# Optimization experiments

Hardware: AMD Instinct MI355X
Metric: run time of the kernel (lower is better)

## Reference

```python
import jax, jax.numpy as jnp
import numpy as np

DIM = 512
HEADS = 8
LANDMARKS = 64


def setup_inputs() -> dict:
    key = jax.random.key(0)
    ks = jax.random.split(key, 9)
    B, N, C = 2, 16384, DIM
    s = 0.02
    return {
        "x": jax.random.normal(ks[0], (B, N, C), dtype=jnp.float32),
        "wq": jax.random.normal(ks[1], (C, C), dtype=jnp.float32) * s,
        "bq": jnp.zeros((C,), dtype=jnp.float32),
        "wk": jax.random.normal(ks[2], (C, C), dtype=jnp.float32) * s,
        "bk": jnp.zeros((C,), dtype=jnp.float32),
        "wv": jax.random.normal(ks[3], (C, C), dtype=jnp.float32) * s,
        "bv": jnp.zeros((C,), dtype=jnp.float32),
        "wo": jax.random.normal(ks[4], (C, C), dtype=jnp.float32) * s,
        "bo": jnp.zeros((C,), dtype=jnp.float32),
    }


def _to_heads(x, H):
    B, N, C = x.shape
    return x.reshape(B, N, H, C // H).transpose(0, 2, 1, 3)  # (B,H,N,hd)


def reference(x, wq, bq, wk, bk, wv, bv, wo, bo):
    B, N, C = x.shape
    H = HEADS
    hd = C // H
    scale = hd ** (-0.5)
    m = min(LANDMARKS, N)

    q = _to_heads(x @ wq.T + bq, H) * scale  # (B,H,N,hd)
    k = _to_heads(x @ wk.T + bk, H)
    v = _to_heads(x @ wv.T + bv, H)

    if N <= m * 2:
        attn = jax.nn.softmax(jnp.einsum("bhnd,bhkd->bhnk", q, k), axis=-1)
        out = jnp.einsum("bhnk,bhkd->bhnd", attn, v)
    else:
        seg = (N + m - 1) // m
        pad = seg * m - N
        if pad > 0:
            q_p = jnp.pad(q, ((0, 0), (0, 0), (0, pad), (0, 0)))
            k_p = jnp.pad(k, ((0, 0), (0, 0), (0, pad), (0, 0)))
        else:
            q_p, k_p = q, k
        # landmarks: mean over consecutive segments of length seg (zero-pad included, as in torch)
        q_land = q_p.reshape(B, H, m, seg, hd).mean(3)  # (B,H,m,hd)
        k_land = k_p.reshape(B, H, m, seg, hd).mean(3)

        ker1 = jax.nn.softmax(jnp.einsum("bhnd,bhmd->bhnm", q, k_land), axis=-1)  # (B,H,N,m)
        ker2 = jax.nn.softmax(jnp.einsum("bhld,bhmd->bhlm", q_land, k_land), axis=-1)  # (B,H,m,m)
        ker3 = jax.nn.softmax(jnp.einsum("bhmd,bhnd->bhmn", q_land, k), axis=-1)  # (B,H,m,N)
        ker2_inv = jnp.linalg.pinv(ker2)  # (B,H,m,m)

        kv = jnp.einsum("bhmn,bhnd->bhmd", ker3, v)  # (B,H,m,hd)
        out = jnp.einsum("bhnm,bhmd->bhnd", ker1, ker2_inv @ kv)

    out = out.transpose(0, 2, 1, 3).reshape(B, N, C)
    return out @ wo.T + bo
```

## Files before the change

kernel.cpp:

```cpp
#include <hip/hip_runtime.h>
#include <stdint.h>


constexpr int B_   = 2;
constexpr int N_   = 16384;
constexpr int C_   = 512;
constexpr int H_   = 8;
constexpr int HD_  = 64;
constexpr int LM_  = 64;
constexpr int SEG_ = 256;
constexpr int BH_  = 16;
constexpr int NCH_ = 16;
constexpr int NPART_ = 64;
constexpr int SW1_ = 3;
constexpr int SW2_ = 2;

#define RCOND_ (640.0 * 1.1920928955078125e-07)

typedef unsigned short ushort4_t __attribute__((ext_vector_type(4)));
typedef unsigned short ushort8_t __attribute__((ext_vector_type(8)));
typedef __bf16 bf16x8 __attribute__((ext_vector_type(8)));
typedef float f32x4 __attribute__((ext_vector_type(4)));

__device__ inline float bf2f(unsigned short u) {
  union { unsigned int i; float f; } x; x.i = ((unsigned int)u) << 16; return x.f;
}
__device__ inline unsigned short f2bf(float f) {
  union { float f; unsigned int i; } x; x.f = f;
  unsigned int lsb = (x.i >> 16) & 1;
  return (unsigned short)((x.i + 0x7fffu + lsb) >> 16);
}
__device__ inline bf16x8 ld_bf8(const unsigned short* p) { return *(const bf16x8*)p; }

__device__ __forceinline__ void gload_lds16(const unsigned short* gsrc, unsigned short* ldst) {
  __builtin_amdgcn_global_load_lds((const __attribute__((address_space(1))) void*)gsrc,
                                   (__attribute__((address_space(3))) void*)ldst, 16, 0, 0);
}

__global__ __launch_bounds__(256) void cvt_bf16_kernel(const float* __restrict__ src,
                                                       unsigned short* __restrict__ dst,
                                                       int n8) {
  int i = (blockIdx.x * 256 + threadIdx.x);
  if (i >= n8) return;
  const float* s = src + (size_t)i * 8;
  float4 x0 = *(const float4*)(s);
  float4 x1 = *(const float4*)(s + 4);
  ushort8_t u;
  u[0] = f2bf(x0.x); u[1] = f2bf(x0.y); u[2] = f2bf(x0.z); u[3] = f2bf(x0.w);
  u[4] = f2bf(x1.x); u[5] = f2bf(x1.y); u[6] = f2bf(x1.z); u[7] = f2bf(x1.w);
  *(ushort8_t*)(dst + (size_t)i * 8) = u;
}

__global__ __launch_bounds__(256) void seg_mean_kernel(const float* __restrict__ x,
                                                       float* __restrict__ xbar) {
  int bl = blockIdx.x;
  int b = bl / LM_, l = bl % LM_;
  int t = threadIdx.x;
  int c4 = t & 127;
  int rh = t >> 7;
  const float* xp = x + ((size_t)b * N_ + (size_t)l * SEG_) * C_;
  float4 s = make_float4(0.f, 0.f, 0.f, 0.f);
  for (int r = rh * 128; r < rh * 128 + 128; ++r) {
    float4 v = *(const float4*)(xp + (size_t)r * C_ + c4 * 4);
    s.x += v.x; s.y += v.y; s.z += v.z; s.w += v.w;
  }
  __shared__ float red[2][512];
  *(float4*)&red[rh][c4 * 4] = s;
  __syncthreads();
  if (rh == 0) {
    float4 a = *(float4*)&red[0][c4 * 4];
    float4 c = *(float4*)&red[1][c4 * 4];
    const float invs = 1.0f / SEG_;
    float4 o;
    o.x = (a.x + c.x) * invs; o.y = (a.y + c.y) * invs;
    o.z = (a.z + c.z) * invs; o.w = (a.w + c.w) * invs;
    *(float4*)(xbar + (size_t)bl * C_ + c4 * 4) = o;
  }
}

__global__ __launch_bounds__(256) void land_gemm_kernel(const float* __restrict__ xbar,
                                                        const float* __restrict__ wq,
                                                        const float* __restrict__ bq,
                                                        const float* __restrict__ wk,
                                                        const float* __restrict__ bk,
                                                        float* __restrict__ qland,
                                                        float* __restrict__ kland,
                                                        unsigned short* __restrict__ qlbh,
                                                        unsigned short* __restrict__ qlbl,
                                                        unsigned short* __restrict__ klb) {
  __shared__ float As[32][68];
  __shared__ float Ws[32][68];
  int which = blockIdx.x >> 1;
  int row0 = (blockIdx.x & 1) * 64;
  int col0 = blockIdx.y * 64;
  const float* A = xbar;
  const float* W = which ? wk : wq;
  const float* bias = which ? bk : bq;
  float scale = which ? 1.0f : 0.125f;
  float* out = which ? kland : qland;
  int tid = threadIdx.x;
  int tm = tid >> 4, tn = tid & 15;
  float acc[4][4] = {};
  for (int k0 = 0; k0 < C_; k0 += 32) {
#pragma unroll
    for (int i = 0; i < 2; ++i) {
      int s = tid + i * 256;
      int r = s >> 3;
      int kg = (s & 7) << 2;
      float4 av = *(const float4*)(A + (size_t)(row0 + r) * C_ + k0 + kg);
      As[kg + 0][r] = av.x; As[kg + 1][r] = av.y;
      As[kg + 2][r] = av.z; As[kg + 3][r] = av.w;
      float4 wv = *(const float4*)(W + (size_t)(col0 + r) * C_ + k0 + kg);
      Ws[kg + 0][r] = wv.x; Ws[kg + 1][r] = wv.y;
      Ws[kg + 2][r] = wv.z; Ws[kg + 3][r] = wv.w;
    }
    __syncthreads();
#pragma unroll
    for (int kk = 0; kk < 32; ++kk) {
      float4 a = *(const float4*)&As[kk][tm * 4];
      float4 b = *(const float4*)&Ws[kk][tn * 4];
      float av[4] = {a.x, a.y, a.z, a.w};
      float bv[4] = {b.x, b.y, b.z, b.w};
#pragma unroll
      for (int i = 0; i < 4; ++i)
#pragma unroll
        for (int j = 0; j < 4; ++j) acc[i][j] += av[i] * bv[j];
    }
    __syncthreads();
  }
#pragma unroll
  for (int i = 0; i < 4; ++i) {
    int row = row0 + tm * 4 + i;
    int d0 = tn * 4;
    float o4[4];
#pragma unroll
    for (int j = 0; j < 4; ++j) o4[j] = (acc[i][j] + bias[col0 + d0 + j]) * scale;
    int b = row / LM_, n = row % LM_;
    int h = col0 >> 6;
    size_t idx = (((size_t)(b * H_ + h) * LM_) + n) * HD_ + d0;
    float4 o; o.x = o4[0]; o.y = o4[1]; o.z = o4[2]; o.w = o4[3];
    *(float4*)(out + idx) = o;
    if (which == 0) {
      ushort4_t uh, ul;
#pragma unroll
      for (int j = 0; j < 4; ++j) {
        unsigned short hbits = f2bf(o4[j]);
        uh[j] = hbits;
        ul[j] = f2bf(o4[j] - bf2f(hbits));
      }
      *(ushort4_t*)(qlbh + idx) = uh;
      *(ushort4_t*)(qlbl + idx) = ul;
    } else {
      ushort4_t uk;
#pragma unroll
      for (int j = 0; j < 4; ++j) uk[j] = f2bf(o4[j]);
      *(ushort4_t*)(klb + idx) = uk;
    }
  }
}

__device__ __forceinline__ void mfma_gemm_body(const float* __restrict__ A,
                                               const float* __restrict__ W,
                                               const float* __restrict__ bias,
                                               unsigned short* __restrict__ out,
                                               float scale, int omode,
                                               int row0, int col0,
                                               unsigned short* Xs, unsigned short* Ws,
                                               int tid) {
  int wid = tid >> 6, lane = tid & 63;
  int wr = wid >> 1, wc = wid & 1;
  f32x4 acc[4][4] = {};
  int srow = tid >> 1;
  int sk = (tid & 1) * 16;
  const float* wpbase = W + (size_t)(col0 + srow) * C_ + sk;
  const float* apbase = A + (size_t)(row0 + srow) * C_ + sk;
  unsigned short* xdst = &Xs[srow * 32 + sk];
  unsigned short* wdst = &Ws[srow * 32 + sk];

  for (int k0 = 0; k0 < C_; k0 += 32) {
    __syncthreads();
    {
      float4 x0 = *(const float4*)(apbase + k0);
      float4 x1 = *(const float4*)(apbase + k0 + 4);
      float4 x2 = *(const float4*)(apbase + k0 + 8);
      float4 x3 = *(const float4*)(apbase + k0 + 12);
      ushort8_t u0, u1;
      u0[0] = f2bf(x0.x); u0[1] = f2bf(x0.y); u0[2] = f2bf(x0.z); u0[3] = f2bf(x0.w);
      u0[4] = f2bf(x1.x); u0[5] = f2bf(x1.y); u0[6] = f2bf(x1.z); u0[7] = f2bf(x1.w);
      u1[0] = f2bf(x2.x); u1[1] = f2bf(x2.y); u1[2] = f2bf(x2.z); u1[3] = f2bf(x2.w);
      u1[4] = f2bf(x3.x); u1[5] = f2bf(x3.y); u1[6] = f2bf(x3.z); u1[7] = f2bf(x3.w);
      *(ushort8_t*)(xdst) = u0;
      *(ushort8_t*)(xdst + 8) = u1;
    }
    {
      float4 w0 = *(const float4*)(wpbase + k0);
      float4 w1 = *(const float4*)(wpbase + k0 + 4);
      float4 w2 = *(const float4*)(wpbase + k0 + 8);
      float4 w3 = *(const float4*)(wpbase + k0 + 12);
      ushort8_t u0, u1;
      u0[0] = f2bf(w0.x); u0[1] = f2bf(w0.y); u0[2] = f2bf(w0.z); u0[3] = f2bf(w0.w);
      u0[4] = f2bf(w1.x); u0[5] = f2bf(w1.y); u0[6] = f2bf(w1.z); u0[7] = f2bf(w1.w);
      u1[0] = f2bf(w2.x); u1[1] = f2bf(w2.y); u1[2] = f2bf(w2.z); u1[3] = f2bf(w2.w);
      u1[4] = f2bf(w3.x); u1[5] = f2bf(w3.y); u1[6] = f2bf(w3.z); u1[7] = f2bf(w3.w);
      *(ushort8_t*)(wdst) = u0;
      *(ushort8_t*)(wdst + 8) = u1;
    }
    __syncthreads();
    bf16x8 af[4], bfr[4];
#pragma unroll
    for (int m = 0; m < 4; ++m)
      af[m] = *(bf16x8*)&Xs[(wr * 64 + m * 16 + (lane & 15)) * 32 + (lane >> 4) * 8];
#pragma unroll
    for (int n = 0; n < 4; ++n)
      bfr[n] = *(bf16x8*)&Ws[(wc * 64 + n * 16 + (lane & 15)) * 32 + (lane >> 4) * 8];
#pragma unroll
    for (int m = 0; m < 4; ++m)
#pragma unroll
      for (int n = 0; n < 4; ++n)
        acc[m][n] = __builtin_amdgcn_mfma_f32_16x16x32_bf16(af[m], bfr[n], acc[m][n], 0, 0, 0);
  }

#pragma unroll
  for (int m = 0; m < 4; ++m) {
    int rbase = row0 + wr * 64 + m * 16 + (lane >> 4) * 4;
#pragma unroll
    for (int n = 0; n < 4; ++n) {
      int c = col0 + wc * 64 + n * 16 + (lane & 15);
      float bc = bias[c];
      if (omode == 2) {
        int b = rbase >> 14, nn = rbase & 16383;
        int h = c >> 6, d = c & 63;
        ushort4_t u;
#pragma unroll
        for (int rg = 0; rg < 4; ++rg) u[rg] = f2bf((acc[m][n][rg] + bc) * scale);
        *(ushort4_t*)(out + ((size_t)(b * H_ + h) * HD_ + d) * N_ + nn) = u;
      } else {
#pragma unroll
        for (int rg = 0; rg < 4; ++rg) {
          float val = (acc[m][n][rg] + bc) * scale;
          int r = rbase + rg;
          int b = r >> 14, nn = r & 16383, h = c >> 6, d = c & 63;
          out[(((size_t)(b * H_ + h) * N_) + nn) * HD_ + d] = f2bf(val);
        }
      }
    }
  }
}

__device__ __forceinline__ void svd_sweeps(float a[16], float v[16], char* smemraw,
                                           int w, int lane, int nsweeps) {
  float (*Ac)[68]    = (float(*)[68])(smemraw);
  float (*Vc)[68]    = (float(*)[68])(smemraw + 17408);
  float (*pg)[4][64] = (float(*)[4][64])(smemraw + 34816);
  float (*pa4)[64]   = (float(*)[64])(smemraw + 36864);
  const int r0 = w * 16;
  *(float4*)&Ac[lane][r0 + 0]  = make_float4(a[0], a[1], a[2], a[3]);
  *(float4*)&Ac[lane][r0 + 4]  = make_float4(a[4], a[5], a[6], a[7]);
  *(float4*)&Ac[lane][r0 + 8]  = make_float4(a[8], a[9], a[10], a[11]);
  *(float4*)&Ac[lane][r0 + 12] = make_float4(a[12], a[13], a[14], a[15]);
  *(float4*)&Vc[lane][r0 + 0]  = make_float4(v[0], v[1], v[2], v[3]);
  *(float4*)&Vc[lane][r0 + 4]  = make_float4(v[4], v[5], v[6], v[7]);
  *(float4*)&Vc[lane][r0 + 8]  = make_float4(v[8], v[9], v[10], v[11]);
  *(float4*)&Vc[lane][r0 + 12] = make_float4(v[12], v[13], v[14], v[15]);

  for (int sweep = 0; sweep < nsweeps; ++sweep) {
    float p0 = 0.f, p1 = 0.f;
#pragma unroll
    for (int k = 0; k < 16; k += 2) { p0 = fmaf(a[k], a[k], p0); p1 = fmaf(a[k + 1], a[k + 1], p1); }
    pa4[w][lane] = p0 + p1;
    __syncthreads();
    float alpha = (pa4[0][lane] + pa4[1][lane]) + (pa4[2][lane] + pa4[3][lane]);
    for (int mask = 1; mask < 64; ++mask) {
      int buf = mask & 1;
      int partner = lane ^ mask;
      bool lower = lane < partner;
      float beta = __shfl_xor(alpha, mask);
      float4 o0 = *(float4*)&Ac[partner][r0 + 0];
      float4 o1 = *(float4*)&Ac[partner][r0 + 4];
      float4 o2 = *(float4*)&Ac[partner][r0 + 8];
      float4 o3 = *(float4*)&Ac[partner][r0 + 12];
      float o[16] = {o0.x, o0.y, o0.z, o0.w, o1.x, o1.y, o1.z, o1.w,
                     o2.x, o2.y, o2.z, o2.w, o3.x, o3.y, o3.z, o3.w};
      float g0 = 0.f, g1 = 0.f;
#pragma unroll
      for (int k = 0; k < 16; k += 2) { g0 = fmaf(a[k], o[k], g0); g1 = fmaf(a[k + 1], o[k + 1], g1); }
      pg[buf][w][lane] = g0 + g1;
      __syncthreads();
      float gamma = (pg[buf][0][lane] + pg[buf][1][lane]) + (pg[buf][2][lane] + pg[buf][3][lane]);
      bool need = (gamma * gamma > 1e-12f * alpha * beta);
      if (__any(need)) {
        float4 q0 = *(float4*)&Vc[partner][r0 + 0];
        float4 q1 = *(float4*)&Vc[partner][r0 + 4];
        float4 q2 = *(float4*)&Vc[partner][r0 + 8];
        float4 q3 = *(float4*)&Vc[partner][r0 + 12];
        float ov[16] = {q0.x, q0.y, q0.z, q0.w, q1.x, q1.y, q1.z, q1.w,
                        q2.x, q2.y, q2.z, q2.w, q3.x, q3.y, q3.z, q3.w};
        float ap = lower ? alpha : beta;
        float aq = lower ? beta : alpha;
        float c = 1.f, s = 0.f;
        if (need) {
          float tau = (aq - ap) / (2.f * gamma);
          float t = copysignf(1.f, tau) / (fabsf(tau) + sqrtf(fmaf(tau, tau, 1.f)));
          c = rsqrtf(fmaf(t, t, 1.f));
          s = t * c;
        }
        float sm = lower ? -s : s;
#pragma unroll
        for (int k = 0; k < 16; ++k) a[k] = fmaf(sm, o[k], c * a[k]);
#pragma unroll
        for (int k = 0; k < 16; ++k) v[k] = fmaf(sm, ov[k], c * v[k]);
        float twocsg = 2.f * c * s * gamma;
        alpha = fmaf(c * c, alpha, fmaf(s * s, beta, lower ? -twocsg : twocsg));
        *(float4*)&Ac[lane][r0 + 0]  = make_float4(a[0], a[1], a[2], a[3]);
        *(float4*)&Ac[lane][r0 + 4]  = make_float4(a[4], a[5], a[6], a[7]);
        *(float4*)&Ac[lane][r0 + 8]  = make_float4(a[8], a[9], a[10], a[11]);
        *(float4*)&Ac[lane][r0 + 12] = make_float4(a[12], a[13], a[14], a[15]);
        *(float4*)&Vc[lane][r0 + 0]  = make_float4(v[0], v[1], v[2], v[3]);
        *(float4*)&Vc[lane][r0 + 4]  = make_float4(v[4], v[5], v[6], v[7]);
        *(float4*)&Vc[lane][r0 + 8]  = make_float4(v[8], v[9], v[10], v[11]);
        *(float4*)&Vc[lane][r0 + 12] = make_float4(v[12], v[13], v[14], v[15]);
      }
    }
  }
}

__device__ void svd_phase1(const float* __restrict__ qland, const float* __restrict__ kland,
                           float* __restrict__ asave, float* __restrict__ vsave,
                           int bh, char* smemraw, int tid) {
  __builtin_amdgcn_s_setprio(3);
  float (*qlS)[65] = (float(*)[65])(smemraw);
  float (*klS)[65] = (float(*)[65])(smemraw + 16640);
  for (int i = 0; i < 4; ++i) {
    int s = tid + i * 256;
    int r = s >> 4, d4 = (s & 15) << 2;
    *(float4*)&qlS[r][d4] = *(const float4*)(qland + ((size_t)bh * 64 + r) * 64 + d4);
    *(float4*)&klS[r][d4] = *(const float4*)(kland + ((size_t)bh * 64 + r) * 64 + d4);
  }
  __syncthreads();
  int w = tid >> 6, lane = tid & 63;
  float a[16], v[16];
#pragma unroll
  for (int k = 0; k < 16; ++k) {
    int row = w * 16 + k;
    float acc = 0.f;
#pragma unroll
    for (int d4 = 0; d4 < 64; d4 += 4) {
      float4 qv = *(float4*)&qlS[row][d4];
      float4 kv = *(float4*)&klS[lane][d4];
      acc += qv.x * kv.x + qv.y * kv.y + qv.z * kv.z + qv.w * kv.w;
    }
    float e = expf(acc);
    float rs = e;
#pragma unroll
    for (int m = 1; m < 64; m <<= 1) rs += __shfl_xor(rs, m);
    a[k] = e * (1.f / rs);
  }
#pragma unroll
  for (int k = 0; k < 16; ++k) v[k] = (w * 16 + k == lane) ? 1.f : 0.f;
  __syncthreads();
  svd_sweeps(a, v, smemraw, w, lane, SW1_);
#pragma unroll
  for (int k = 0; k < 16; ++k) {
    asave[((size_t)bh * 64 + w * 16 + k) * 64 + lane] = a[k];
    vsave[((size_t)bh * 64 + w * 16 + k) * 64 + lane] = v[k];
  }
  __builtin_amdgcn_s_setprio(0);
}

__device__ void svd_phase2(const float* __restrict__ asave, const float* __restrict__ vsave,
                           float* __restrict__ pinv, int bh, char* smemraw, int tid) {
  __builtin_amdgcn_s_setprio(3);
  double (*ps2)[64]  = (double(*)[64])(smemraw + 37888);
  float (*vsL)[65]   = (float(*)[65])(smemraw);
  float (*wasL)[65]  = (float(*)[65])(smemraw + 16640);
  int w = tid >> 6, lane = tid & 63;
  float a[16], v[16];
#pragma unroll
  for (int k = 0; k < 16; ++k) {
    a[k] = asave[((size_t)bh * 64 + w * 16 + k) * 64 + lane];
    v[k] = vsave[((size_t)bh * 64 + w * 16 + k) * 64 + lane];
  }
  svd_sweeps(a, v, smemraw, w, lane, SW2_);

  double psig = 0.0;
#pragma unroll
  for (int k = 0; k < 16; ++k) psig += (double)a[k] * (double)a[k];
  ps2[w][lane] = psig;
  __syncthreads();
  double sig2 = (ps2[0][lane] + ps2[1][lane]) + (ps2[2][lane] + ps2[3][lane]);
  double smax = sig2;
#pragma unroll
  for (int m = 1; m < 64; m <<= 1) smax = fmax(smax, __shfl_xor(smax, m));
  double cutoff2 = smax * (RCOND_ * RCOND_);
  float wgt = (sig2 > cutoff2) ? (float)(1.0 / sig2) : 0.f;

#pragma unroll
  for (int k = 0; k < 16; ++k) {
    vsL[lane][w * 16 + k] = v[k];
    wasL[lane][w * 16 + k] = wgt * a[k];
  }
  __syncthreads();
  int i = tid >> 2;
  int j0 = (tid & 3) * 16;
  float acc[16] = {};
  for (int r = 0; r < 64; ++r) {
    float vv = vsL[r][i];
#pragma unroll
    for (int jj = 0; jj < 16; ++jj) acc[jj] = fmaf(vv, wasL[r][j0 + jj], acc[jj]);
  }
#pragma unroll
  for (int jj = 0; jj < 16; jj += 4) {
    float4 ovv = make_float4(acc[jj], acc[jj + 1], acc[jj + 2], acc[jj + 3]);
    *(float4*)(pinv + ((size_t)bh * 64 + i) * 64 + j0 + jj) = ovv;
  }
  __builtin_amdgcn_s_setprio(0);
}

__global__ __launch_bounds__(256) void fused1_kernel(
    const float* __restrict__ x,
    const float* __restrict__ wq, const float* __restrict__ bq,
    const float* __restrict__ wk, const float* __restrict__ bk,
    const float* __restrict__ wv, const float* __restrict__ bv,
    unsigned short* __restrict__ q4, unsigned short* __restrict__ k4,
    unsigned short* __restrict__ vt,
    const float* __restrict__ qland, const float* __restrict__ kland,
    float* __restrict__ asave, float* __restrict__ vsave) {
  __shared__ __align__(16) char smem[37888];
  int tid = threadIdx.x;
  int blk = blockIdx.x;
  if (blk < 16) { svd_phase1(qland, kland, asave, vsave, blk, smem, tid); return; }
  int g = blk - 16;
  int which = g >> 10;
  int sub = g & 1023;
  int row0 = (sub >> 2) * 128;
  int col0 = (sub & 3) * 128;
  unsigned short* Xs = (unsigned short*)smem;
  unsigned short* Ws = Xs + 128 * 32;
  if (which == 0)
    mfma_gemm_body(x, wq, bq, q4, 0.125f, 1, row0, col0, Xs, Ws, tid);
  else if (which == 1)
    mfma_gemm_body(x, wk, bk, k4, 1.0f, 1, row0, col0, Xs, Ws, tid);
  else
    mfma_gemm_body(x, wv, bv, vt, 1.0f, 2, row0, col0, Xs, Ws, tid);
}

__device__ void ker3kv_body(const unsigned short* __restrict__ qlh,
                            const unsigned short* __restrict__ qll,
                            const unsigned short* __restrict__ k4,
                            const unsigned short* __restrict__ vt,
                            float* __restrict__ pacc,
                            float* __restrict__ pacc0,
                            float* __restrict__ ps,
                            int bh, int ch, char* smemraw, int tid) {
  int w = tid >> 6, lane = tid & 63;
  int part = ch * 4 + w;
  int lrow = lane & 15, lgrp = lane >> 4;
  unsigned short* myP = (unsigned short*)smemraw + w * 64 * 72;

  bf16x8 qah[4][2], qal[4][2];
#pragma unroll
  for (int mf = 0; mf < 4; ++mf)
#pragma unroll
    for (int ks = 0; ks < 2; ++ks) {
      size_t off = ((size_t)bh * 64 + mf * 16 + lrow) * 64 + ks * 32 + lgrp * 8;
      qah[mf][ks] = ld_bf8(qlh + off);
      qal[mf][ks] = ld_bf8(qll + off);
    }
  bf16x8 onesf;
#pragma unroll
  for (int j = 0; j < 8; ++j) onesf[j] = (__bf16)1.0f;

  f32x4 kvacc[4][4] = {};
  f32x4 oneacc[4] = {};
  f32x4 ssum[4] = {};

  for (int sub = 0; sub < 4; ++sub) {
    int n0 = ch * 1024 + w * 256 + sub * 64;
    f32x4 sacc[4][4] = {};
#pragma unroll
    for (int ks = 0; ks < 2; ++ks) {
#pragma unroll
      for (int nf = 0; nf < 4; ++nf) {
        bf16x8 kb = ld_bf8(k4 + ((size_t)bh * N_ + n0 + nf * 16 + lrow) * 64 + ks * 32 + lgrp * 8);
#pragma unroll
        for (int mf = 0; mf < 4; ++mf) {
          sacc[mf][nf] = __builtin_amdgcn_mfma_f32_16x16x32_bf16(qah[mf][ks], kb, sacc[mf][nf], 0, 0, 0);
          sacc[mf][nf] = __builtin_amdgcn_mfma_f32_16x16x32_bf16(qal[mf][ks], kb, sacc[mf][nf], 0, 0, 0);
        }
      }
    }
#pragma unroll
    for (int mf = 0; mf < 4; ++mf) {
#pragma unroll
      for (int nf = 0; nf < 4; ++nf) {
#pragma unroll
        for (int r = 0; r < 4; ++r) {
          float pd = expf(sacc[mf][nf][r]) - 1.0f;
          ssum[mf][r] += pd;
          myP[(mf * 16 + lgrp * 4 + r) * 72 + nf * 16 + lrow] = f2bf(pd);
        }
      }
    }
#pragma unroll
    for (int ks = 0; ks < 2; ++ks) {
      bf16x8 pa[4];
#pragma unroll
      for (int mf = 0; mf < 4; ++mf)
        pa[mf] = ld_bf8(myP + (mf * 16 + lrow) * 72 + ks * 32 + lgrp * 8);
#pragma unroll
      for (int nf = 0; nf < 4; ++nf) {
        bf16x8 vb = ld_bf8(vt + ((size_t)bh * 64 + nf * 16 + lrow) * N_ + n0 + ks * 32 + lgrp * 8);
#pragma unroll
        for (int mf = 0; mf < 4; ++mf)
          kvacc[mf][nf] = __builtin_amdgcn_mfma_f32_16x16x32_bf16(pa[mf], vb, kvacc[mf][nf], 0, 0, 0);
        oneacc[nf] = __builtin_amdgcn_mfma_f32_16x16x32_bf16(onesf, vb, oneacc[nf], 0, 0, 0);
      }
    }
  }
#pragma unroll
  for (int mf = 0; mf < 4; ++mf)
#pragma unroll
    for (int m = 1; m < 16; m <<= 1)
#pragma unroll
      for (int r = 0; r < 4; ++r) ssum[mf][r] += __shfl_xor(ssum[mf][r], m);

  size_t pb = (((size_t)bh * NPART_ + part) * 64) * 64;
#pragma unroll
  for (int mf = 0; mf < 4; ++mf)
#pragma unroll
    for (int nf = 0; nf < 4; ++nf)
#pragma unroll
      for (int r = 0; r < 4; ++r)
        pacc[pb + (size_t)(mf * 16 + lgrp * 4 + r) * 64 + nf * 16 + lrow] = kvacc[mf][nf][r];
  if (lrow == 0) {
#pragma unroll
    for (int mf = 0; mf < 4; ++mf)
#pragma unroll
      for (int r = 0; r < 4; ++r)
        ps[((size_t)bh * NPART_ + part) * 64 + mf * 16 + lgrp * 4 + r] = ssum[mf][r];
  }
  if (lgrp == 0) {
#pragma unroll
    for (int nf = 0; nf < 4; ++nf)
      pacc0[((size_t)bh * NPART_ + part) * 64 + nf * 16 + lrow] = oneacc[nf][0];
  }
}

__global__ __launch_bounds__(256, 1) void fused2_kernel(
    const unsigned short* __restrict__ qlh,
    const unsigned short* __restrict__ qll,
    const unsigned short* __restrict__ k4,
    const unsigned short* __restrict__ vt,
    float* __restrict__ pacc, float* __restrict__ pacc0, float* __restrict__ ps,
    const float* __restrict__ asave, const float* __restrict__ vsave,
    float* __restrict__ pinv) {
  __shared__ __align__(16) char smem[39936];
  int tid = threadIdx.x;
  int blk = blockIdx.x;
  if (blk < 16) { svd_phase2(asave, vsave, pinv, blk, smem, tid); return; }
  int g = blk - 16;
  int bh = g >> 4, ch = g & 15;
  ker3kv_body(qlh, qll, k4, vt, pacc, pacc0, ps, bh, ch, smem, tid);
}

__global__ __launch_bounds__(256) void kv_combine_kernel(const float* __restrict__ pacc,
                                                         const float* __restrict__ pacc0,
                                                         const float* __restrict__ ps,
                                                         float* __restrict__ kv) {
  int bh = blockIdx.y;
  int lm = blockIdx.x * 16 + (threadIdx.x >> 4);
  int d4 = (threadIdx.x & 15) * 4;
  float s = 16384.f;
  for (int part = 0; part < NPART_; ++part) s += ps[((size_t)bh * NPART_ + part) * 64 + lm];
  float4 a = make_float4(0.f, 0.f, 0.f, 0.f);
  for (int part = 0; part < NPART_; ++part) {
    float4 c0 = *(const float4*)&pacc0[((size_t)bh * NPART_ + part) * 64 + d4];
    float4 v = *(const float4*)&pacc[(((size_t)bh * NPART_ + part) * 64 + lm) * 64 + d4];
    a.x += c0.x + v.x; a.y += c0.y + v.y; a.z += c0.z + v.z; a.w += c0.w + v.w;
  }
  float inv = 1.f / s;
  float4 o = make_float4(a.x * inv, a.y * inv, a.z * inv, a.w * inv);
  *(float4*)(kv + ((size_t)bh * 64 + lm) * 64 + d4) = o;
}

__global__ __launch_bounds__(256) void mmat_kernel(const float* __restrict__ pinv,
                                                   const float* __restrict__ kv,
                                                   unsigned short* __restrict__ mtbh,
                                                   unsigned short* __restrict__ mtbl,
                                                   float* __restrict__ msum) {
  int bh = blockIdx.x;
  int tid = threadIdx.x;
  __shared__ float kvs[64][68];
  __shared__ double pcsd[64];
  for (int i = 0; i < 4; ++i) {
    int s = tid + i * 256;
    int r = s >> 4, d4 = (s & 15) << 2;
    *(float4*)&kvs[r][d4] = *(const float4*)(kv + ((size_t)bh * 64 + r) * 64 + d4);
  }
  if (tid < 64) {
    double s = 0.0;
    for (int l = 0; l < 64; ++l) s += (double)pinv[((size_t)bh * 64 + l) * 64 + tid];
    pcsd[tid] = s;
  }
  __syncthreads();
  int l = tid >> 2, t = tid & 3;
  double o[16] = {};
  for (int j = 0; j < 64; ++j) {
    double pv = (double)pinv[((size_t)bh * 64 + l) * 64 + j];
#pragma unroll
    for (int i = 0; i < 16; ++i) o[i] += pv * (double)kvs[j][t * 16 + i];
  }
#pragma unroll
  for (int i = 0; i < 16; ++i) {
    float f = (float)o[i];
    unsigned short hi = f2bf(f);
    float lo = f - bf2f(hi);
    int d = t * 16 + i;
    mtbh[((size_t)bh * 64 + d) * 64 + l] = hi;
    mtbl[((size_t)bh * 64 + d) * 64 + l] = f2bf(lo);
  }
  if (tid < 64) {
    double m = 0.0;
    for (int j = 0; j < 64; ++j) m += pcsd[j] * (double)kvs[j][tid];
    msum[(size_t)bh * 64 + tid] = (float)(m * (1.0 / 64.0));
  }
}

__global__ __launch_bounds__(256, 1) void ker1out_mfma_kernel(
    const unsigned short* __restrict__ q4,
    const unsigned short* __restrict__ klb,
    const unsigned short* __restrict__ mtbh,
    const unsigned short* __restrict__ mtbl,
    const float* __restrict__ msum,
    unsigned short* __restrict__ outh) {
  int bh = blockIdx.y, tile = blockIdx.x;
  int b = bh >> 3, h = bh & 7;
  int tid = threadIdx.x, w = tid >> 6, lane = tid & 63;
  int lrow = lane & 15, lgrp = lane >> 4;
  int tok0 = tile * 256 + w * 64;
  __shared__ __align__(16) unsigned short Pl[4][64 * 72];
  unsigned short* myP = &Pl[w][0];

  f32x4 sacc[4][4] = {};
#pragma unroll
  for (int ks = 0; ks < 2; ++ks) {
    bf16x8 kb[4];
#pragma unroll
    for (int nf = 0; nf < 4; ++nf)
      kb[nf] = ld_bf8(klb + ((size_t)bh * 64 + nf * 16 + lrow) * 64 + ks * 32 + lgrp * 8);
#pragma unroll
    for (int mf = 0; mf < 4; ++mf) {
      bf16x8 qa = ld_bf8(q4 + ((size_t)bh * N_ + tok0 + mf * 16 + lrow) * 64 + ks * 32 + lgrp * 8);
#pragma unroll
      for (int nf = 0; nf < 4; ++nf)
        sacc[mf][nf] = __builtin_amdgcn_mfma_f32_16x16x32_bf16(qa, kb[nf], sacc[mf][nf], 0, 0, 0);
    }
  }
  f32x4 ssum[4] = {};
#pragma unroll
  for (int mf = 0; mf < 4; ++mf)
#pragma unroll
    for (int nf = 0; nf < 4; ++nf)
#pragma unroll
      for (int r = 0; r < 4; ++r) {
        sacc[mf][nf][r] = expf(sacc[mf][nf][r]);
        ssum[mf][r] += sacc[mf][nf][r];
      }
#pragma unroll
  for (int mf = 0; mf < 4; ++mf)
#pragma unroll
    for (int m = 1; m < 16; m <<= 1)
#pragma unroll
      for (int r = 0; r < 4; ++r) ssum[mf][r] += __shfl_xor(ssum[mf][r], m);
#pragma unroll
  for (int mf = 0; mf < 4; ++mf) {
    f32x4 inv;
#pragma unroll
    for (int r = 0; r < 4; ++r) inv[r] = 1.f / ssum[mf][r];
#pragma unroll
    for (int nf = 0; nf < 4; ++nf)
#pragma unroll
      for (int r = 0; r < 4; ++r) {
        float pdev = fmaf(sacc[mf][nf][r], inv[r], -0.015625f);
        myP[(mf * 16 + lgrp * 4 + r) * 72 + nf * 16 + lrow] = f2bf(pdev);
      }
  }

  f32x4 oacc[4][4] = {};
#pragma unroll
  for (int ks = 0; ks < 2; ++ks) {
    bf16x8 pa[4];
#pragma unroll
    for (int mf = 0; mf < 4; ++mf)
      pa[mf] = ld_bf8(myP + (mf * 16 + lrow) * 72 + ks * 32 + lgrp * 8);
#pragma unroll
    for (int nf = 0; nf < 4; ++nf) {
      bf16x8 mh = ld_bf8(mtbh + ((size_t)bh * 64 + nf * 16 + lrow) * 64 + ks * 32 + lgrp * 8);
      bf16x8 ml = ld_bf8(mtbl + ((size_t)bh * 64 + nf * 16 + lrow) * 64 + ks * 32 + lgrp * 8);
#pragma unroll
      for (int mf = 0; mf < 4; ++mf) {
        oacc[mf][nf] = __builtin_amdgcn_mfma_f32_16x16x32_bf16(pa[mf], mh, oacc[mf][nf], 0, 0, 0);
        oacc[mf][nf] = __builtin_amdgcn_mfma_f32_16x16x32_bf16(pa[mf], ml, oacc[mf][nf], 0, 0, 0);
      }
    }
  }
#pragma unroll
  for (int nf = 0; nf < 4; ++nf) {
    float ms = msum[(size_t)bh * 64 + nf * 16 + lrow];
#pragma unroll
    for (int mf = 0; mf < 4; ++mf)
#pragma unroll
      for (int r = 0; r < 4; ++r) {
        int tok = tok0 + mf * 16 + lgrp * 4 + r;
        int d = nf * 16 + lrow;
        outh[((size_t)b * N_ + tok) * C_ + h * HD_ + d] = f2bf(oacc[mf][nf][r] + ms);
      }
  }
}

__global__ __launch_bounds__(256) void oproj_kernel(const unsigned short* __restrict__ outh,
                                                    const unsigned short* __restrict__ wob,
                                                    const float* __restrict__ bo,
                                                    float* __restrict__ out) {
  __shared__ __align__(16) unsigned short Xs[128 * 32];
  __shared__ __align__(16) unsigned short Ws[128 * 32];
  int tid = threadIdx.x;
  int w = tid >> 6, lane = tid & 63;
  int wr = w >> 1, wc = w & 1;
  int row0 = blockIdx.x * 128, col0 = blockIdx.y * 128;
  f32x4 acc[4][4] = {};

  for (int k0 = 0; k0 < C_; k0 += 32) {
    __syncthreads();
#pragma unroll
    for (int i = 0; i < 2; ++i) {
      const unsigned short* gx = outh + (size_t)(row0 + w * 32 + i * 16 + (lane >> 2)) * C_ + k0 + (lane & 3) * 8;
      gload_lds16(gx, &Xs[(w * 32 + i * 16) * 32]);
      const unsigned short* gw = wob + (size_t)(col0 + w * 32 + i * 16 + (lane >> 2)) * C_ + k0 + (lane & 3) * 8;
      gload_lds16(gw, &Ws[(w * 32 + i * 16) * 32]);
    }
    __syncthreads();
    bf16x8 af[4], bfr[4];
#pragma unroll
    for (int m = 0; m < 4; ++m)
      af[m] = *(bf16x8*)&Xs[(wr * 64 + m * 16 + (lane & 15)) * 32 + (lane >> 4) * 8];
#pragma unroll
    for (int n = 0; n < 4; ++n)
      bfr[n] = *(bf16x8*)&Ws[(wc * 64 + n * 16 + (lane & 15)) * 32 + (lane >> 4) * 8];
#pragma unroll
    for (int m = 0; m < 4; ++m)
#pragma unroll
      for (int n = 0; n < 4; ++n)
        acc[m][n] = __builtin_amdgcn_mfma_f32_16x16x32_bf16(af[m], bfr[n], acc[m][n], 0, 0, 0);
  }

#pragma unroll
  for (int m = 0; m < 4; ++m) {
    int rbase = row0 + wr * 64 + m * 16 + (lane >> 4) * 4;
#pragma unroll
    for (int n = 0; n < 4; ++n) {
      int c = col0 + wc * 64 + n * 16 + (lane & 15);
      float bc = bo[c];
#pragma unroll
      for (int rg = 0; rg < 4; ++rg)
        out[(size_t)(rbase + rg) * C_ + c] = acc[m][n][rg] + bc;
    }
  }
}

extern "C" void kernel_launch(void* const* d_in, const int* in_sizes, int n_in,
                              void* d_out, int out_size, void* d_ws, size_t ws_size,
                              hipStream_t stream) {
  const float* x  = (const float*)d_in[0];
  const float* wq = (const float*)d_in[1];
  const float* bq = (const float*)d_in[2];
  const float* wk = (const float*)d_in[3];
  const float* bk = (const float*)d_in[4];
  const float* wv = (const float*)d_in[5];
  const float* bv = (const float*)d_in[6];
  const float* wo = (const float*)d_in[7];
  const float* bo = (const float*)d_in[8];
  float* out = (float*)d_out;

  char* base = (char*)d_ws;
  const size_t QKV = (size_t)BH_ * N_ * HD_;
  unsigned short* q4 = (unsigned short*)base;
  unsigned short* k4 = (unsigned short*)(base + QKV * 2);
  unsigned short* vt = (unsigned short*)(base + QKV * 4);
  unsigned short* outh = (unsigned short*)(base + QKV * 2);
  char* sp = base + QKV * 6;
  float* pacc  = (float*)sp; sp += (size_t)BH_ * NPART_ * 64 * 64 * 4;
  float* pacc0 = (float*)sp; sp += (size_t)BH_ * NPART_ * 64 * 4;
  float* ps    = (float*)sp; sp += (size_t)BH_ * NPART_ * 64 * 4;
  float* xbar  = (float*)sp; sp += (size_t)B_ * LM_ * C_ * 4;
  float* qland = (float*)sp; sp += (size_t)BH_ * LM_ * HD_ * 4;
  float* kland = (float*)sp; sp += (size_t)BH_ * LM_ * HD_ * 4;
  unsigned short* qlbh = (unsigned short*)sp; sp += (size_t)BH_ * LM_ * HD_ * 2;
  unsigned short* qlbl = (unsigned short*)sp; sp += (size_t)BH_ * LM_ * HD_ * 2;
  unsigned short* klb  = (unsigned short*)sp; sp += (size_t)BH_ * LM_ * HD_ * 2;
  float* pinv  = (float*)sp; sp += (size_t)BH_ * LM_ * LM_ * 4;
  float* kvb   = (float*)sp; sp += (size_t)BH_ * LM_ * HD_ * 4;
  unsigned short* mtbh = (unsigned short*)sp; sp += (size_t)BH_ * LM_ * HD_ * 2;
  unsigned short* mtbl = (unsigned short*)sp; sp += (size_t)BH_ * LM_ * HD_ * 2;
  float* msum  = (float*)sp; sp += (size_t)BH_ * HD_ * 4;
  float* asave = (float*)sp; sp += (size_t)BH_ * LM_ * LM_ * 4;
  float* vsave = (float*)sp; sp += (size_t)BH_ * LM_ * LM_ * 4;
  unsigned short* wob = (unsigned short*)sp; sp += (size_t)C_ * C_ * 2;

  const int W8 = (C_ * C_) / 8;

  cvt_bf16_kernel<<<W8 / 256, 256, 0, stream>>>(wo, wob, W8);

  seg_mean_kernel<<<B_ * LM_, 256, 0, stream>>>(x, xbar);
  dim3 gl(4, 8);
  land_gemm_kernel<<<gl, 256, 0, stream>>>(xbar, wq, bq, wk, bk,
                                           qland, kland, qlbh, qlbl, klb);

  fused1_kernel<<<16 + 3 * 1024, 256, 0, stream>>>(
      x, wq, bq, wk, bk, wv, bv, q4, k4, vt, qland, kland, asave, vsave);

  fused2_kernel<<<16 + NCH_ * BH_, 256, 0, stream>>>(
      qlbh, qlbl, k4, vt, pacc, pacc0, ps, asave, vsave, pinv);

  dim3 g7(4, BH_);
  kv_combine_kernel<<<g7, 256, 0, stream>>>(pacc, pacc0, ps, kvb);
  mmat_kernel<<<BH_, 256, 0, stream>>>(pinv, kvb, mtbh, mtbl, msum);

  dim3 g9(N_ / 256, BH_);
  ker1out_mfma_kernel<<<g9, 256, 0, stream>>>(q4, klb, mtbh, mtbl, msum, outh);

  dim3 g10(B_ * N_ / 128, C_ / 128);
  oproj_kernel<<<g10, 256, 0, stream>>>(outh, wob, bo, out);
}
```

Measured before the change: 415.0 us.

## Pre-convert x and QKV weights to bf16 and use LDS DMA loads in projections

```diff
diff --git a/kernel.cpp b/kernel.cpp
--- a/kernel.cpp
+++ b/kernel.cpp
@@ -37,11 +37,18 @@
                                    (__attribute__((address_space(3))) void*)ldst, 16, 0, 0);
 }
 
-__global__ __launch_bounds__(256) void cvt_bf16_kernel(const float* __restrict__ src,
-                                                       unsigned short* __restrict__ dst,
-                                                       int n8) {
-  int i = (blockIdx.x * 256 + threadIdx.x);
-  if (i >= n8) return;
+__global__ __launch_bounds__(256) void cvt_w4_kernel(const float* __restrict__ wq,
+                                                     const float* __restrict__ wk,
+                                                     const float* __restrict__ wv,
+                                                     const float* __restrict__ wo,
+                                                     unsigned short* __restrict__ dq,
+                                                     unsigned short* __restrict__ dk,
+                                                     unsigned short* __restrict__ dv,
+                                                     unsigned short* __restrict__ dwo) {
+  int which = blockIdx.y;
+  const float* src = which == 0 ? wq : which == 1 ? wk : which == 2 ? wv : wo;
+  unsigned short* dst = which == 0 ? dq : which == 1 ? dk : which == 2 ? dv : dwo;
+  int i = blockIdx.x * 256 + threadIdx.x;
   const float* s = src + (size_t)i * 8;
   float4 x0 = *(const float4*)(s);
   float4 x1 = *(const float4*)(s + 4);
@@ -52,17 +59,22 @@
 }
 
 __global__ __launch_bounds__(256) void seg_mean_kernel(const float* __restrict__ x,
-                                                       float* __restrict__ xbar) {
+                                                       float* __restrict__ xbar,
+                                                       unsigned short* __restrict__ xb) {
   int bl = blockIdx.x;
   int b = bl / LM_, l = bl % LM_;
   int t = threadIdx.x;
   int c4 = t & 127;
   int rh = t >> 7;
-  const float* xp = x + ((size_t)b * N_ + (size_t)l * SEG_) * C_;
+  const size_t rowbase = (size_t)b * N_ + (size_t)l * SEG_;
+  const float* xp = x + rowbase * C_;
   float4 s = make_float4(0.f, 0.f, 0.f, 0.f);
   for (int r = rh * 128; r < rh * 128 + 128; ++r) {
     float4 v = *(const float4*)(xp + (size_t)r * C_ + c4 * 4);
     s.x += v.x; s.y += v.y; s.z += v.z; s.w += v.w;
+    ushort4_t u;
+    u[0] = f2bf(v.x); u[1] = f2bf(v.y); u[2] = f2bf(v.z); u[3] = f2bf(v.w);
+    *(ushort4_t*)(xb + (rowbase + r) * C_ + c4 * 4) = u;
   }
   __shared__ float red[2][512];
   *(float4*)&red[rh][c4 * 4] = s;
@@ -159,51 +171,26 @@
   }
 }
 
-__device__ __forceinline__ void mfma_gemm_body(const float* __restrict__ A,
-                                               const float* __restrict__ W,
-                                               const float* __restrict__ bias,
-                                               unsigned short* __restrict__ out,
-                                               float scale, int omode,
-                                               int row0, int col0,
-                                               unsigned short* Xs, unsigned short* Ws,
-                                               int tid) {
-  int wid = tid >> 6, lane = tid & 63;
-  int wr = wid >> 1, wc = wid & 1;
+__device__ __forceinline__ void dma_gemm_body(const unsigned short* __restrict__ A,
+                                              const unsigned short* __restrict__ W,
+                                              const float* __restrict__ bias,
+                                              void* __restrict__ out,
+                                              float scale, int omode,
+                                              int row0, int col0,
+                                              unsigned short* Xs, unsigned short* Wl,
+                                              int tid) {
+  int w = tid >> 6, lane = tid & 63;
+  int wr = w >> 1, wc = w & 1;
   f32x4 acc[4][4] = {};
-  int srow = tid >> 1;
-  int sk = (tid & 1) * 16;
-  const float* wpbase = W + (size_t)(col0 + srow) * C_ + sk;
-  const float* apbase = A + (size_t)(row0 + srow) * C_ + sk;
-  unsigned short* xdst = &Xs[srow * 32 + sk];
-  unsigned short* wdst = &Ws[srow * 32 + sk];
 
   for (int k0 = 0; k0 < C_; k0 += 32) {
     __syncthreads();
-    {
-      float4 x0 = *(const float4*)(apbase + k0);
-      float4 x1 = *(const float4*)(apbase + k0 + 4);
-      float4 x2 = *(const float4*)(apbase + k0 + 8);
-      float4 x3 = *(const float4*)(apbase + k0 + 12);
-      ushort8_t u0, u1;
-      u0[0] = f2bf(x0.x); u0[1] = f2bf(x0.y); u0[2] = f2bf(x0.z); u0[3] = f2bf(x0.w);
-      u0[4] = f2bf(x1.x); u0[5] = f2bf(x1.y); u0[6] = f2bf(x1.z); u0[7] = f2bf(x1.w);
-      u1[0] = f2bf(x2.x); u1[1] = f2bf(x2.y); u1[2] = f2bf(x2.z); u1[3] = f2bf(x2.w);
-      u1[4] = f2bf(x3.x); u1[5] = f2bf(x3.y); u1[6] = f2bf(x3.z); u1[7] = f2bf(x3.w);
-      *(ushort8_t*)(xdst) = u0;
-      *(ushort8_t*)(xdst + 8) = u1;
-    }
-    {
-      float4 w0 = *(const float4*)(wpbase + k0);
-      float4 w1 = *(const float4*)(wpbase + k0 + 4);
-      float4 w2 = *(const float4*)(wpbase + k0 + 8);
-      float4 w3 = *(const float4*)(wpbase + k0 + 12);
-      ushort8_t u0, u1;
-      u0[0] = f2bf(w0.x); u0[1] = f2bf(w0.y); u0[2] = f2bf(w0.z); u0[3] = f2bf(w0.w);
-      u0[4] = f2bf(w1.x); u0[5] = f2bf(w1.y); u0[6] = f2bf(w1.z); u0[7] = f2bf(w1.w);
-      u1[0] = f2bf(w2.x); u1[1] = f2bf(w2.y); u1[2] = f2bf(w2.z); u1[3] = f2bf(w2.w);
-      u1[4] = f2bf(w3.x); u1[5] = f2bf(w3.y); u1[6] = f2bf(w3.z); u1[7] = f2bf(w3.w);
-      *(ushort8_t*)(wdst) = u0;
-      *(ushort8_t*)(wdst + 8) = u1;
+#pragma unroll
+    for (int i = 0; i < 2; ++i) {
+      const unsigned short* gx = A + (size_t)(row0 + w * 32 + i * 16 + (lane >> 2)) * C_ + k0 + (lane & 3) * 8;
+      gload_lds16(gx, &Xs[(w * 32 + i * 16) * 32]);
+      const unsigned short* gw = W + (size_t)(col0 + w * 32 + i * 16 + (lane >> 2)) * C_ + k0 + (lane & 3) * 8;
+      gload_lds16(gw, &Wl[(w * 32 + i * 16) * 32]);
     }
     __syncthreads();
     bf16x8 af[4], bfr[4];
@@ -212,7 +199,7 @@
       af[m] = *(bf16x8*)&Xs[(wr * 64 + m * 16 + (lane & 15)) * 32 + (lane >> 4) * 8];
 #pragma unroll
     for (int n = 0; n < 4; ++n)
-      bfr[n] = *(bf16x8*)&Ws[(wc * 64 + n * 16 + (lane & 15)) * 32 + (lane >> 4) * 8];
+      bfr[n] = *(bf16x8*)&Wl[(wc * 64 + n * 16 + (lane & 15)) * 32 + (lane >> 4) * 8];
 #pragma unroll
     for (int m = 0; m < 4; ++m)
 #pragma unroll
@@ -227,20 +214,24 @@
     for (int n = 0; n < 4; ++n) {
       int c = col0 + wc * 64 + n * 16 + (lane & 15);
       float bc = bias[c];
-      if (omode == 2) {
+      if (omode == 0) {
+#pragma unroll
+        for (int rg = 0; rg < 4; ++rg)
+          ((float*)out)[(size_t)(rbase + rg) * C_ + c] = acc[m][n][rg] + bc;
+      } else if (omode == 2) {
         int b = rbase >> 14, nn = rbase & 16383;
         int h = c >> 6, d = c & 63;
         ushort4_t u;
 #pragma unroll
         for (int rg = 0; rg < 4; ++rg) u[rg] = f2bf((acc[m][n][rg] + bc) * scale);
-        *(ushort4_t*)(out + ((size_t)(b * H_ + h) * HD_ + d) * N_ + nn) = u;
+        *(ushort4_t*)((unsigned short*)out + ((size_t)(b * H_ + h) * HD_ + d) * N_ + nn) = u;
       } else {
 #pragma unroll
         for (int rg = 0; rg < 4; ++rg) {
           float val = (acc[m][n][rg] + bc) * scale;
           int r = rbase + rg;
           int b = r >> 14, nn = r & 16383, h = c >> 6, d = c & 63;
-          out[(((size_t)(b * H_ + h) * N_) + nn) * HD_ + d] = f2bf(val);
+          ((unsigned short*)out)[(((size_t)(b * H_ + h) * N_) + nn) * HD_ + d] = f2bf(val);
         }
       }
     }
@@ -417,10 +408,10 @@
 }
 
 __global__ __launch_bounds__(256) void fused1_kernel(
-    const float* __restrict__ x,
-    const float* __restrict__ wq, const float* __restrict__ bq,
-    const float* __restrict__ wk, const float* __restrict__ bk,
-    const float* __restrict__ wv, const float* __restrict__ bv,
+    const unsigned short* __restrict__ xb,
+    const unsigned short* __restrict__ wqb, const float* __restrict__ bq,
+    const unsigned short* __restrict__ wkb, const float* __restrict__ bk,
+    const unsigned short* __restrict__ wvb, const float* __restrict__ bv,
     unsigned short* __restrict__ q4, unsigned short* __restrict__ k4,
     unsigned short* __restrict__ vt,
     const float* __restrict__ qland, const float* __restrict__ kland,
@@ -435,13 +426,13 @@
   int row0 = (sub >> 2) * 128;
   int col0 = (sub & 3) * 128;
   unsigned short* Xs = (unsigned short*)smem;
-  unsigned short* Ws = Xs + 128 * 32;
+  unsigned short* Wl = Xs + 128 * 32;
   if (which == 0)
-    mfma_gemm_body(x, wq, bq, q4, 0.125f, 1, row0, col0, Xs, Ws, tid);
+    dma_gemm_body(xb, wqb, bq, q4, 0.125f, 1, row0, col0, Xs, Wl, tid);
   else if (which == 1)
-    mfma_gemm_body(x, wk, bk, k4, 1.0f, 1, row0, col0, Xs, Ws, tid);
+    dma_gemm_body(xb, wkb, bk, k4, 1.0f, 1, row0, col0, Xs, Wl, tid);
   else
-    mfma_gemm_body(x, wv, bv, vt, 1.0f, 2, row0, col0, Xs, Ws, tid);
+    dma_gemm_body(xb, wvb, bv, vt, 1.0f, 2, row0, col0, Xs, Wl, tid);
 }
 
 __device__ void ker3kv_body(const unsigned short* __restrict__ qlh,
@@ -723,49 +714,9 @@
                                                     const float* __restrict__ bo,
                                                     float* __restrict__ out) {
   __shared__ __align__(16) unsigned short Xs[128 * 32];
-  __shared__ __align__(16) unsigned short Ws[128 * 32];
-  int tid = threadIdx.x;
-  int w = tid >> 6, lane = tid & 63;
-  int wr = w >> 1, wc = w & 1;
-  int row0 = blockIdx.x * 128, col0 = blockIdx.y * 128;
-  f32x4 acc[4][4] = {};
-
-  for (int k0 = 0; k0 < C_; k0 += 32) {
-    __syncthreads();
-#pragma unroll
-    for (int i = 0; i < 2; ++i) {
-      const unsigned short* gx = outh + (size_t)(row0 + w * 32 + i * 16 + (lane >> 2)) * C_ + k0 + (lane & 3) * 8;
-      gload_lds16(gx, &Xs[(w * 32 + i * 16) * 32]);
-      const unsigned short* gw = wob + (size_t)(col0 + w * 32 + i * 16 + (lane >> 2)) * C_ + k0 + (lane & 3) * 8;
-      gload_lds16(gw, &Ws[(w * 32 + i * 16) * 32]);
-    }
-    __syncthreads();
-    bf16x8 af[4], bfr[4];
-#pragma unroll
-    for (int m = 0; m < 4; ++m)
-      af[m] = *(bf16x8*)&Xs[(wr * 64 + m * 16 + (lane & 15)) * 32 + (lane >> 4) * 8];
-#pragma unroll
-    for (int n = 0; n < 4; ++n)
-      bfr[n] = *(bf16x8*)&Ws[(wc * 64 + n * 16 + (lane & 15)) * 32 + (lane >> 4) * 8];
-#pragma unroll
-    for (int m = 0; m < 4; ++m)
-#pragma unroll
-      for (int n = 0; n < 4; ++n)
-        acc[m][n] = __builtin_amdgcn_mfma_f32_16x16x32_bf16(af[m], bfr[n], acc[m][n], 0, 0, 0);
-  }
-
-#pragma unroll
-  for (int m = 0; m < 4; ++m) {
-    int rbase = row0 + wr * 64 + m * 16 + (lane >> 4) * 4;
-#pragma unroll
-    for (int n = 0; n < 4; ++n) {
-      int c = col0 + wc * 64 + n * 16 + (lane & 15);
-      float bc = bo[c];
-#pragma unroll
-      for (int rg = 0; rg < 4; ++rg)
-        out[(size_t)(rbase + rg) * C_ + c] = acc[m][n][rg] + bc;
-    }
-  }
+  __shared__ __align__(16) unsigned short Wl[128 * 32];
+  dma_gemm_body(outh, wob, bo, out, 1.0f, 0, blockIdx.x * 128, blockIdx.y * 128,
+                Xs, Wl, threadIdx.x);
 }
 
 extern "C" void kernel_launch(void* const* d_in, const int* in_sizes, int n_in,
@@ -806,18 +757,24 @@
   float* asave = (float*)sp; sp += (size_t)BH_ * LM_ * LM_ * 4;
   float* vsave = (float*)sp; sp += (size_t)BH_ * LM_ * LM_ * 4;
   unsigned short* wob = (unsigned short*)sp; sp += (size_t)C_ * C_ * 2;
+  unsigned short* wqb = (unsigned short*)sp; sp += (size_t)C_ * C_ * 2;
+  unsigned short* wkb = (unsigned short*)sp; sp += (size_t)C_ * C_ * 2;
+  unsigned short* wvb = (unsigned short*)sp; sp += (size_t)C_ * C_ * 2;
+
+  unsigned short* xb = (unsigned short*)d_out;
 
   const int W8 = (C_ * C_) / 8;
 
-  cvt_bf16_kernel<<<W8 / 256, 256, 0, stream>>>(wo, wob, W8);
-
-  seg_mean_kernel<<<B_ * LM_, 256, 0, stream>>>(x, xbar);
+  dim3 gc(W8 / 256, 4);
+  cvt_w4_kernel<<<gc, 256, 0, stream>>>(wq, wk, wv, wo, wqb, wkb, wvb, wob);
+
+  seg_mean_kernel<<<B_ * LM_, 256, 0, stream>>>(x, xbar, xb);
   dim3 gl(4, 8);
   land_gemm_kernel<<<gl, 256, 0, stream>>>(xbar, wq, bq, wk, bk,
                                            qland, kland, qlbh, qlbl, klb);
 
   fused1_kernel<<<16 + 3 * 1024, 256, 0, stream>>>(
-      x, wq, bq, wk, bk, wv, bv, q4, k4, vt, qland, kland, asave, vsave);
+      xb, wqb, bq, wkb, bk, wvb, bv, q4, k4, vt, qland, kland, asave, vsave);
 
   fused2_kernel<<<16 + NCH_ * BH_, 256, 0, stream>>>(
       qlbh, qlbl, k4, vt, pacc, pacc0, ps, asave, vsave, pinv);
```

After: 447.2 us. 1.08x slower.
